# Performance work log

Hardware: AMD Instinct MI355X
Metric: run time of the kernel (lower is better)

## Reference

```python
import jax, jax.numpy as jnp
import numpy as np

EPS = 1e-5  # torch GroupNorm default eps


def _pairwise_sqdist(x, y):
    # squared euclidean distance matrix, clamped at 0 for numerical safety
    d = (jnp.sum(x * x, -1)[:, None] + jnp.sum(y * y, -1)[None, :]
         - 2.0 * (x @ y.T))
    return jnp.maximum(d, 0.0)


def _pc_normalize(ref, src):
    # jointly center and scale both clouds to the unit sphere
    pts = jnp.concatenate([ref, src], axis=0)
    centroid = pts.mean(axis=0, keepdims=True)
    pts = pts - centroid
    m = jnp.max(jnp.linalg.norm(pts, axis=1))
    pts = pts / m
    n_ref = ref.shape[0]
    return pts[:n_ref], pts[n_ref:]


def _group_norm(x, gamma, beta, groups):
    N, C = x.shape
    xg = x.reshape(N, groups, C // groups)
    mean = xg.mean(-1, keepdims=True)
    var = jnp.mean((xg - mean) ** 2, -1, keepdims=True)
    xn = ((xg - mean) / jnp.sqrt(var + EPS)).reshape(N, C)
    return xn * gamma + beta


def setup_inputs() -> dict:
    key = jax.random.key(0)
    ks = jax.random.split(key, 8)
    N_ref, N_src, D = 128, 128, 256
    points_c = jax.random.normal(ks[0], (N_ref + N_src, 3), jnp.float32)
    ref_feats = jax.random.normal(ks[1], (N_ref, D), jnp.float32)
    src_feats = jax.random.normal(ks[2], (N_src, D), jnp.float32)
    # normalized features, as the '_norm' names suggest
    ref_feats = ref_feats / jnp.linalg.norm(ref_feats, axis=-1, keepdims=True)
    src_feats = src_feats / jnp.linalg.norm(src_feats, axis=-1, keepdims=True)
    # a valid rigid transform: random rotation + small translation
    A = jax.random.normal(ks[3], (3, 3), jnp.float32)
    Q, _ = jnp.linalg.qr(A)
    trans = jnp.eye(4, dtype=jnp.float32)
    trans = trans.at[:3, :3].set(Q)
    trans = trans.at[:3, 3].set(jax.random.normal(ks[4], (3,), jnp.float32) * 0.1)
    s = 1.0 / np.sqrt(512)
    return {
        'points_c': points_c,
        'ref_feats_c_norm': ref_feats,
        'src_feats_c_norm': src_feats,
        'trans': trans,
        'W1': jax.random.normal(ks[5], (256, 512), jnp.float32) * s,
        'b1': jnp.zeros((256,), jnp.float32),
        'g1': jnp.ones((256,), jnp.float32),
        'bt1': jnp.zeros((256,), jnp.float32),
        'W2': jax.random.normal(ks[6], (128, 256), jnp.float32) * (1.0 / np.sqrt(256)),
        'b2': jnp.zeros((128,), jnp.float32),
        'g2': jnp.ones((128,), jnp.float32),
        'bt2': jnp.zeros((128,), jnp.float32),
        'W3': jax.random.normal(ks[7], (2, 128), jnp.float32) * (1.0 / np.sqrt(128)),
        'b3': jnp.zeros((2,), jnp.float32),
        'ref_length': 128,
    }


def reference(points_c, ref_feats_c_norm, src_feats_c_norm, trans,
              W1, b1, g1, bt1, W2, b2, g2, bt2, W3, b3, ref_length):
    GROUPS = 8
    ref_points = points_c[:ref_length]
    src_points = points_c[ref_length:]
    # apply rigid transform to src points
    src_points = src_points @ trans[:3, :3].T + trans[:3, 3]
    ref_n, src_n = _pc_normalize(ref_points, src_points)

    dist_mat = jnp.exp(-_pairwise_sqdist(ref_n, src_n))  # [Nr, Ns]
    match_idx_ref = jnp.argmax(dist_mat, axis=1)
    match_idx_src = jnp.argmax(dist_mat, axis=0)
    min_dist_ref = jnp.max(dist_mat, axis=1)
    min_dist_src = jnp.max(dist_mat, axis=0)

    feat_score_mat = ref_feats_c_norm @ src_feats_c_norm.T  # [Nr, Ns]
    feat_match_idx_ref = jnp.argmax(feat_score_mat, axis=1)
    feat_match_idx_src = jnp.argmax(feat_score_mat, axis=0)
    feat_match_ref = jnp.max(feat_score_mat, axis=1)
    feat_match_src = jnp.max(feat_score_mat, axis=0)

    r_idx = jnp.arange(feat_score_mat.shape[0])
    c_idx = jnp.arange(feat_score_mat.shape[1])
    feat_score_ref = feat_score_mat[r_idx, match_idx_ref]
    feat_score_src = feat_score_mat[match_idx_src, c_idx]
    dist_ref = dist_mat[r_idx, feat_match_idx_ref]
    dist_src = dist_mat[feat_match_idx_src, c_idx]

    min_dist = jnp.concatenate([min_dist_ref, min_dist_src])
    feat_score = jnp.concatenate([feat_score_ref, feat_score_src])
    perm_d = jnp.argsort(-min_dist)  # descending sort
    d_m = min_dist[perm_d] * feat_score[perm_d]

    match_feat = jnp.concatenate([feat_match_ref, feat_match_src])
    match_dist = jnp.concatenate([dist_ref, dist_src])
    perm_f = jnp.argsort(-match_feat)
    m_d = match_dist[perm_f] * match_feat[perm_f]

    geo_out = jnp.concatenate([d_m, m_d])[None, :]  # [1, 512]

    h = _group_norm(geo_out @ W1.T + b1, g1, bt1, GROUPS)
    h = jax.nn.relu(h)
    h = _group_norm(h @ W2.T + b2, g2, bt2, GROUPS)
    h = jax.nn.relu(h)
    return h @ W3.T + b3  # [1, num_classes]
```

## Files before the change

### kernel.cpp

```cpp
#include <hip/hip_runtime.h>
#include <math.h>

#define NREF 128
#define NSRC 128
#define DIM  256
#define EPS  1e-5f

__global__ __launch_bounds__(512) void feat_kernel(
    const float* __restrict__ ref_feats,
    const float* __restrict__ src_feats,
    float* __restrict__ feat_mat)
{
    __shared__ __align__(16) float refrow[DIM];
    const int i = blockIdx.x;
    const int t = threadIdx.x;
    if (t < 64) ((float4*)refrow)[t] = ((const float4*)(ref_feats + i * DIM))[t];
    __syncthreads();

    const int w = t >> 6, l = t & 63;
    const float4 r = ((const float4*)refrow)[l];

    for (int m = 0; m < 16; m += 2) {
        const int j0 = w * 16 + m;
        const int j1 = j0 + 1;
        const float4 a0 = ((const float4*)(src_feats + j0 * DIM))[l];
        const float4 a1 = ((const float4*)(src_feats + j1 * DIM))[l];
        float acc0 = a0.x * r.x + a0.y * r.y + a0.z * r.z + a0.w * r.w;
        float acc1 = a1.x * r.x + a1.y * r.y + a1.z * r.z + a1.w * r.w;
        for (int off = 32; off >= 1; off >>= 1) {
            acc0 += __shfl_down(acc0, off);
            acc1 += __shfl_down(acc1, off);
        }
        if (l == 0) {
            feat_mat[i * NSRC + j0] = acc0;
            feat_mat[i * NSRC + j1] = acc1;
        }
    }
}

__global__ __launch_bounds__(1024) void geo_kernel(
    const float* __restrict__ points_c,
    const float* __restrict__ trans,
    const float* __restrict__ feat_mat,
    float* __restrict__ geo_out)
{
    __shared__ float px[256], py[256], pz[256], nsq[256];
    __shared__ float wred[16];
    __shared__ float red[4];
    __shared__ float pvD[1024]; __shared__ int piD[1024];
    __shared__ float pvF[1024]; __shared__ int piF[1024];
    __shared__ float min_dist[256];   __shared__ int match_idx[256];
    __shared__ float match_feat[256]; __shared__ int feat_idx[256];
    __shared__ float feat_score[256], match_dist[256];
    __shared__ int prD[1024]; __shared__ int prF[1024];

    const int t    = threadIdx.x;
    const int wave = t >> 6;
    const int lane = t & 63;

    float x = 0.f, y = 0.f, z = 0.f;
    if (t < 256) {
        x = points_c[3 * t + 0];
        y = points_c[3 * t + 1];
        z = points_c[3 * t + 2];
        if (t >= NREF) {
            float nx = trans[0] * x + trans[1] * y + trans[2]  * z + trans[3];
            float ny = trans[4] * x + trans[5] * y + trans[6]  * z + trans[7];
            float nz = trans[8] * x + trans[9] * y + trans[10] * z + trans[11];
            x = nx; y = ny; z = nz;
        }
        float sx = x, sy = y, sz = z;
        for (int off = 32; off >= 1; off >>= 1) {
            sx += __shfl_down(sx, off);
            sy += __shfl_down(sy, off);
            sz += __shfl_down(sz, off);
        }
        if (lane == 0) {
            wred[wave]     = sx;
            wred[4 + wave] = sy;
            wred[8 + wave] = sz;
        }
    }
    __syncthreads();
    if (t == 0) {
        red[0] = (wred[0] + wred[1] + wred[2] + wred[3]) * (1.0f / 256.0f);
        red[1] = (wred[4] + wred[5] + wred[6] + wred[7]) * (1.0f / 256.0f);
        red[2] = (wred[8] + wred[9] + wred[10] + wred[11]) * (1.0f / 256.0f);
    }
    __syncthreads();

    if (t < 256) {
        x -= red[0]; y -= red[1]; z -= red[2];
        float n = x * x + y * y + z * z;
        float mx = n;
        for (int off = 32; off >= 1; off >>= 1)
            mx = fmaxf(mx, __shfl_down(mx, off));
        if (lane == 0) wred[wave] = mx;
    }
    __syncthreads();
    if (t == 0)
        red[3] = 1.0f / sqrtf(fmaxf(fmaxf(wred[0], wred[1]), fmaxf(wred[2], wred[3])));
    __syncthreads();
    if (t < 256) {
        const float inv = red[3];
        x *= inv; y *= inv; z *= inv;
        px[t] = x; py[t] = y; pz[t] = z;
        nsq[t] = x * x + y * y + z * z;
    }
    __syncthreads();

    {
        const int rc = t & 255, q = t >> 8;
        float bdv = -1.f; int bdi = 0;
        float bfv = -2.f; int bfi = 0;
        if (rc < 128) {
            const int i = rc;
            for (int m = 0; m < 32; ++m) {
                const int j = q * 32 + m;
                float d = nsq[i] + nsq[128 + j]
                        - 2.0f * (px[i] * px[128 + j] + py[i] * py[128 + j] + pz[i] * pz[128 + j]);
                d = fmaxf(d, 0.f);
                const float v = expf(-d);
                if (v > bdv) { bdv = v; bdi = j; }
                const float f = feat_mat[i * NSRC + j];
                if (f > bfv) { bfv = f; bfi = j; }
            }
        } else {
            const int j = rc - 128;
            for (int m = 0; m < 32; ++m) {
                const int i = q * 32 + m;
                float d = nsq[i] + nsq[128 + j]
                        - 2.0f * (px[i] * px[128 + j] + py[i] * py[128 + j] + pz[i] * pz[128 + j]);
                d = fmaxf(d, 0.f);
                const float v = expf(-d);
                if (v > bdv) { bdv = v; bdi = i; }
                const float f = feat_mat[i * NSRC + j];
                if (f > bfv) { bfv = f; bfi = i; }
            }
        }
        pvD[q * 256 + rc] = bdv; piD[q * 256 + rc] = bdi;
        pvF[q * 256 + rc] = bfv; piF[q * 256 + rc] = bfi;
    }
    __syncthreads();

    if (t < 256) {
        float bv = -1.f; int bi = 0;
        for (int q = 0; q < 4; ++q) {
            const float v = pvD[q * 256 + t];
            if (v > bv) { bv = v; bi = piD[q * 256 + t]; }
        }
        min_dist[t] = bv; match_idx[t] = bi;
        float fv = -2.f; int fi = 0;
        for (int q = 0; q < 4; ++q) {
            const float v = pvF[q * 256 + t];
            if (v > fv) { fv = v; fi = piF[q * 256 + t]; }
        }
        match_feat[t] = fv; feat_idx[t] = fi;
    }
    __syncthreads();

    if (t < 256) {
        if (t < NREF) {
            const int i = t;
            feat_score[t] = feat_mat[i * NSRC + match_idx[t]];
            const int j = feat_idx[t];
            float d = nsq[i] + nsq[128 + j]
                    - 2.0f * (px[i] * px[128 + j] + py[i] * py[128 + j] + pz[i] * pz[128 + j]);
            d = fmaxf(d, 0.f);
            match_dist[t] = expf(-d);
        } else {
            const int j = t - 128;
            feat_score[t] = feat_mat[match_idx[t] * NSRC + j];
            const int i = feat_idx[t];
            float d = nsq[i] + nsq[128 + j]
                    - 2.0f * (px[i] * px[128 + j] + py[i] * py[128 + j] + pz[i] * pz[128 + j]);
            d = fmaxf(d, 0.f);
            match_dist[t] = expf(-d);
        }
    }
    __syncthreads();

    {
        const int e = t & 255, q = t >> 8;
        const float v  = min_dist[e];
        const float wv = match_feat[e];
        int r1 = 0, r2 = 0;
        for (int m = 0; m < 64; ++m) {
            const int j = q * 64 + m;
            const float u  = min_dist[j];
            r1 += (u > v) || (u == v && j < e);
            const float uf = match_feat[j];
            r2 += (uf > wv) || (uf == wv && j < e);
        }
        prD[q * 256 + e] = r1;
        prF[q * 256 + e] = r2;
    }
    __syncthreads();
    if (t < 256) {
        const int r  = prD[t] + prD[256 + t] + prD[512 + t] + prD[768 + t];
        geo_out[r] = min_dist[t] * feat_score[t];
        const int rf = prF[t] + prF[256 + t] + prF[512 + t] + prF[768 + t];
        geo_out[256 + rf] = match_dist[t] * match_feat[t];
    }
}

__global__ __launch_bounds__(64) void mlp1_kernel(
    const float* __restrict__ geo,
    const float* __restrict__ W1, const float* __restrict__ b1,
    float* __restrict__ y1)
{
    const int c = blockIdx.x, l = threadIdx.x;
    const float4 ga = ((const float4*)geo)[l];
    const float4 gb = ((const float4*)geo)[64 + l];
    const float4* __restrict__ wrow = (const float4*)(W1 + c * 512);
    const float4 a = wrow[l];
    const float4 b = wrow[64 + l];
    float acc = a.x * ga.x + a.y * ga.y + a.z * ga.z + a.w * ga.w
              + b.x * gb.x + b.y * gb.y + b.z * gb.z + b.w * gb.w;
    acc += __shfl_down(acc, 32);
    acc += __shfl_down(acc, 16);
    acc += __shfl_down(acc, 8);
    acc += __shfl_down(acc, 4);
    acc += __shfl_down(acc, 2);
    acc += __shfl_down(acc, 1);
    if (l == 0) y1[c] = acc + b1[c];
}

__global__ __launch_bounds__(64) void mlp2_kernel(
    const float* __restrict__ y1,
    const float* __restrict__ g1, const float* __restrict__ bt1,
    const float* __restrict__ W2, const float* __restrict__ b2,
    float* __restrict__ y2)
{
    __shared__ __align__(16) float y1s[256];
    __shared__ float stats[16];
    const int c = blockIdx.x, l = threadIdx.x;
    ((float4*)y1s)[l] = ((const float4*)y1)[l];
    __syncthreads();
    if (l < 8) {
        float s = 0.f;
        for (int k = 0; k < 32; ++k) s += y1s[(l << 5) + k];
        const float mean = s * (1.0f / 32.0f);
        float q = 0.f;
        for (int k = 0; k < 32; ++k) { const float d = y1s[(l << 5) + k] - mean; q += d * d; }
        const float var = q * (1.0f / 32.0f);
        stats[l] = mean;
        stats[8 + l] = rsqrtf(var + EPS);
    }
    __syncthreads();
    const float4 gg = ((const float4*)g1)[l];
    const float4 bb = ((const float4*)bt1)[l];
    const int g = l >> 3;
    const float mean = stats[g], inv = stats[8 + g];
    const float4 yv = ((const float4*)y1s)[l];
    float4 h;
    h.x = fmaxf((yv.x - mean) * inv * gg.x + bb.x, 0.f);
    h.y = fmaxf((yv.y - mean) * inv * gg.y + bb.y, 0.f);
    h.z = fmaxf((yv.z - mean) * inv * gg.z + bb.z, 0.f);
    h.w = fmaxf((yv.w - mean) * inv * gg.w + bb.w, 0.f);
    const float4 wv = ((const float4*)(W2 + c * 256))[l];
    float acc = wv.x * h.x + wv.y * h.y + wv.z * h.z + wv.w * h.w;
    acc += __shfl_down(acc, 32);
    acc += __shfl_down(acc, 16);
    acc += __shfl_down(acc, 8);
    acc += __shfl_down(acc, 4);
    acc += __shfl_down(acc, 2);
    acc += __shfl_down(acc, 1);
    if (l == 0) y2[c] = acc + b2[c];
}

__global__ __launch_bounds__(128) void final_kernel(
    const float* __restrict__ y2,
    const float* __restrict__ g2, const float* __restrict__ bt2,
    const float* __restrict__ W3, const float* __restrict__ b3,
    float* __restrict__ out)
{
    __shared__ float y2s[128], h2[128];
    const int t = threadIdx.x;
    y2s[t] = y2[t];
    __syncthreads();
    {
        const int g = t >> 4;
        float s = 0.f;
        for (int k = 0; k < 16; ++k) s += y2s[(g << 4) + k];
        const float mean = s * (1.0f / 16.0f);
        float q = 0.f;
        for (int k = 0; k < 16; ++k) { const float d = y2s[(g << 4) + k] - mean; q += d * d; }
        const float var = q * (1.0f / 16.0f);
        const float xn = (y2s[t] - mean) * rsqrtf(var + EPS);
        h2[t] = fmaxf(xn * g2[t] + bt2[t], 0.f);
    }
    __syncthreads();
    const int wave = t >> 6, lane = t & 63;
    float acc = W3[wave * 128 + lane] * h2[lane]
              + W3[wave * 128 + 64 + lane] * h2[64 + lane];
    acc += __shfl_down(acc, 32);
    acc += __shfl_down(acc, 16);
    acc += __shfl_down(acc, 8);
    acc += __shfl_down(acc, 4);
    acc += __shfl_down(acc, 2);
    acc += __shfl_down(acc, 1);
    if (lane == 0) out[wave] = acc + b3[wave];
}

extern "C" void kernel_launch(void* const* d_in, const int* in_sizes, int n_in,
                              void* d_out, int out_size, void* d_ws, size_t ws_size,
                              hipStream_t stream)
{
    const float* points_c  = (const float*)d_in[0];
    const float* ref_feats = (const float*)d_in[1];
    const float* src_feats = (const float*)d_in[2];
    const float* trans     = (const float*)d_in[3];
    const float* W1  = (const float*)d_in[4];
    const float* b1  = (const float*)d_in[5];
    const float* g1  = (const float*)d_in[6];
    const float* bt1 = (const float*)d_in[7];
    const float* W2  = (const float*)d_in[8];
    const float* b2  = (const float*)d_in[9];
    const float* g2  = (const float*)d_in[10];
    const float* bt2 = (const float*)d_in[11];
    const float* W3  = (const float*)d_in[12];
    const float* b3  = (const float*)d_in[13];

    float* feat_mat = (float*)d_ws;
    float* geo = feat_mat;
    float* y1  = feat_mat + 512;
    float* y2  = feat_mat + 768;

    feat_kernel<<<dim3(NREF), dim3(512), 0, stream>>>(ref_feats, src_feats, feat_mat);
    geo_kernel<<<dim3(1), dim3(1024), 0, stream>>>(points_c, trans, feat_mat, geo);
    mlp1_kernel<<<dim3(256), dim3(64), 0, stream>>>(geo, W1, b1, y1);
    mlp2_kernel<<<dim3(128), dim3(64), 0, stream>>>(y1, g1, bt1, W2, b2, y2);
    final_kernel<<<dim3(1), dim3(128), 0, stream>>>(y2, g2, bt2, W3, b3, (float*)d_out);
}
```

Baseline: 104.8 us.

## Fuse five kernels into two: per-row/col side kernel and single-block MLP tail

Replaces the feature-matrix kernel, single-block geo kernel and three MLP kernels with two launches. A 256-block side kernel has each block handle one ref row or src column: it recomputes the normalized point cloud, computes its dot products and geometric scores, and reduces the argmaxes locally, so no feature matrix goes through global memory. A single 512-thread tail kernel does the rank-based sort and the whole MLP in shared memory. This cuts launch overhead and intermediate global traffic, at the cost of redundantly recomputing the centroid and scale per block and running the MLP matvecs on one CU.

```diff
diff --git a/kernel.cpp b/kernel.cpp
--- a/kernel.cpp
+++ b/kernel.cpp
@@ -6,57 +6,26 @@
 #define DIM  256
 #define EPS  1e-5f
 
-__global__ __launch_bounds__(512) void feat_kernel(
+__global__ __launch_bounds__(512) void side_kernel(
+    const float* __restrict__ points_c,
+    const float* __restrict__ trans,
     const float* __restrict__ ref_feats,
     const float* __restrict__ src_feats,
-    float* __restrict__ feat_mat)
-{
-    __shared__ __align__(16) float refrow[DIM];
-    const int i = blockIdx.x;
-    const int t = threadIdx.x;
-    if (t < 64) ((float4*)refrow)[t] = ((const float4*)(ref_feats + i * DIM))[t];
-    __syncthreads();
-
-    const int w = t >> 6, l = t & 63;
-    const float4 r = ((const float4*)refrow)[l];
-
-    for (int m = 0; m < 16; m += 2) {
-        const int j0 = w * 16 + m;
-        const int j1 = j0 + 1;
-        const float4 a0 = ((const float4*)(src_feats + j0 * DIM))[l];
-        const float4 a1 = ((const float4*)(src_feats + j1 * DIM))[l];
-        float acc0 = a0.x * r.x + a0.y * r.y + a0.z * r.z + a0.w * r.w;
-        float acc1 = a1.x * r.x + a1.y * r.y + a1.z * r.z + a1.w * r.w;
-        for (int off = 32; off >= 1; off >>= 1) {
-            acc0 += __shfl_down(acc0, off);
-            acc1 += __shfl_down(acc1, off);
-        }
-        if (l == 0) {
-            feat_mat[i * NSRC + j0] = acc0;
-            feat_mat[i * NSRC + j1] = acc1;
-        }
-    }
-}
-
-__global__ __launch_bounds__(1024) void geo_kernel(
-    const float* __restrict__ points_c,
-    const float* __restrict__ trans,
-    const float* __restrict__ feat_mat,
-    float* __restrict__ geo_out)
+    float* __restrict__ arrs)
 {
     __shared__ float px[256], py[256], pz[256], nsq[256];
-    __shared__ float wred[16];
+    __shared__ float wred[12];
     __shared__ float red[4];
-    __shared__ float pvD[1024]; __shared__ int piD[1024];
-    __shared__ float pvF[1024]; __shared__ int piF[1024];
-    __shared__ float min_dist[256];   __shared__ int match_idx[256];
-    __shared__ float match_feat[256]; __shared__ int feat_idx[256];
-    __shared__ float feat_score[256], match_dist[256];
-    __shared__ int prD[1024]; __shared__ int prF[1024];
-
-    const int t    = threadIdx.x;
-    const int wave = t >> 6;
-    const int lane = t & 63;
+    __shared__ float featLds[128];
+    __shared__ float cvD[8]; __shared__ int ciD[8];
+    __shared__ float cvF[8]; __shared__ int ciF[8];
+
+    const int b = blockIdx.x;
+    const int t = threadIdx.x;
+    const int w = t >> 6, l = t & 63;
+
+    const bool isRow = (b < NREF);
+    const int  me    = isRow ? b : (b - NREF);
 
     float x = 0.f, y = 0.f, z = 0.f;
     if (t < 256) {
@@ -69,17 +38,37 @@
             float nz = trans[8] * x + trans[9] * y + trans[10] * z + trans[11];
             x = nx; y = ny; z = nz;
         }
+    }
+
+    const float* __restrict__ myrow = (isRow ? ref_feats : src_feats) + me * DIM;
+    const float4* __restrict__ other = (const float4*)(isRow ? src_feats : ref_feats);
+    const float4 r = ((const float4*)myrow)[l];
+
+    float bfv = -2.f; int bfi = 0;
+    for (int m = 0; m < 16; m += 2) {
+        const int j0 = w * 16 + m, j1 = j0 + 1;
+        const float4 a0 = other[j0 * 64 + l];
+        const float4 a1 = other[j1 * 64 + l];
+        float acc0 = a0.x * r.x + a0.y * r.y + a0.z * r.z + a0.w * r.w;
+        float acc1 = a1.x * r.x + a1.y * r.y + a1.z * r.z + a1.w * r.w;
+        for (int off = 32; off >= 1; off >>= 1) {
+            acc0 += __shfl_xor(acc0, off);
+            acc1 += __shfl_xor(acc1, off);
+        }
+        if (l == 0) { featLds[j0] = acc0; featLds[j1] = acc1; }
+        if (acc0 > bfv) { bfv = acc0; bfi = j0; }
+        if (acc1 > bfv) { bfv = acc1; bfi = j1; }
+    }
+    if (l == 0) { cvF[w] = bfv; ciF[w] = bfi; }
+
+    if (t < 256) {
         float sx = x, sy = y, sz = z;
         for (int off = 32; off >= 1; off >>= 1) {
             sx += __shfl_down(sx, off);
             sy += __shfl_down(sy, off);
             sz += __shfl_down(sz, off);
         }
-        if (lane == 0) {
-            wred[wave]     = sx;
-            wred[4 + wave] = sy;
-            wred[8 + wave] = sz;
-        }
+        if (l == 0) { wred[w] = sx; wred[4 + w] = sy; wred[8 + w] = sz; }
     }
     __syncthreads();
     if (t == 0) {
@@ -88,14 +77,13 @@
         red[2] = (wred[8] + wred[9] + wred[10] + wred[11]) * (1.0f / 256.0f);
     }
     __syncthreads();
-
     if (t < 256) {
         x -= red[0]; y -= red[1]; z -= red[2];
         float n = x * x + y * y + z * z;
         float mx = n;
         for (int off = 32; off >= 1; off >>= 1)
             mx = fmaxf(mx, __shfl_down(mx, off));
-        if (lane == 0) wred[wave] = mx;
+        if (l == 0) wred[w] = mx;
     }
     __syncthreads();
     if (t == 0)
@@ -109,198 +97,163 @@
     }
     __syncthreads();
 
-    {
-        const int rc = t & 255, q = t >> 8;
-        float bdv = -1.f; int bdi = 0;
-        float bfv = -2.f; int bfi = 0;
-        if (rc < 128) {
-            const int i = rc;
-            for (int m = 0; m < 32; ++m) {
-                const int j = q * 32 + m;
-                float d = nsq[i] + nsq[128 + j]
-                        - 2.0f * (px[i] * px[128 + j] + py[i] * py[128 + j] + pz[i] * pz[128 + j]);
-                d = fmaxf(d, 0.f);
-                const float v = expf(-d);
-                if (v > bdv) { bdv = v; bdi = j; }
-                const float f = feat_mat[i * NSRC + j];
-                if (f > bfv) { bfv = f; bfi = j; }
-            }
-        } else {
-            const int j = rc - 128;
-            for (int m = 0; m < 32; ++m) {
-                const int i = q * 32 + m;
-                float d = nsq[i] + nsq[128 + j]
-                        - 2.0f * (px[i] * px[128 + j] + py[i] * py[128 + j] + pz[i] * pz[128 + j]);
-                d = fmaxf(d, 0.f);
-                const float v = expf(-d);
-                if (v > bdv) { bdv = v; bdi = i; }
-                const float f = feat_mat[i * NSRC + j];
-                if (f > bfv) { bfv = f; bfi = i; }
-            }
-        }
-        pvD[q * 256 + rc] = bdv; piD[q * 256 + rc] = bdi;
-        pvF[q * 256 + rc] = bfv; piF[q * 256 + rc] = bfi;
-    }
-    __syncthreads();
-
-    if (t < 256) {
+    float bdv = -1.f; int bdi = 0;
+    for (int m = 0; m < 16; ++m) {
+        const int jj = w * 16 + m;
+        const int i = isRow ? me : jj;
+        const int j = isRow ? jj : me;
+        float d = nsq[i] + nsq[128 + j]
+                - 2.0f * (px[i] * px[128 + j] + py[i] * py[128 + j] + pz[i] * pz[128 + j]);
+        d = fmaxf(d, 0.f);
+        const float v = expf(-d);
+        if (v > bdv) { bdv = v; bdi = jj; }
+    }
+    if (l == 0) { cvD[w] = bdv; ciD[w] = bdi; }
+    __syncthreads();
+
+    if (t == 0) {
         float bv = -1.f; int bi = 0;
-        for (int q = 0; q < 4; ++q) {
-            const float v = pvD[q * 256 + t];
-            if (v > bv) { bv = v; bi = piD[q * 256 + t]; }
-        }
-        min_dist[t] = bv; match_idx[t] = bi;
+        for (int q = 0; q < 8; ++q)
+            if (cvD[q] > bv) { bv = cvD[q]; bi = ciD[q]; }
         float fv = -2.f; int fi = 0;
-        for (int q = 0; q < 4; ++q) {
-            const float v = pvF[q * 256 + t];
-            if (v > fv) { fv = v; fi = piF[q * 256 + t]; }
-        }
-        match_feat[t] = fv; feat_idx[t] = fi;
-    }
-    __syncthreads();
-
-    if (t < 256) {
-        if (t < NREF) {
-            const int i = t;
-            feat_score[t] = feat_mat[i * NSRC + match_idx[t]];
-            const int j = feat_idx[t];
-            float d = nsq[i] + nsq[128 + j]
-                    - 2.0f * (px[i] * px[128 + j] + py[i] * py[128 + j] + pz[i] * pz[128 + j]);
-            d = fmaxf(d, 0.f);
-            match_dist[t] = expf(-d);
-        } else {
-            const int j = t - 128;
-            feat_score[t] = feat_mat[match_idx[t] * NSRC + j];
-            const int i = feat_idx[t];
-            float d = nsq[i] + nsq[128 + j]
-                    - 2.0f * (px[i] * px[128 + j] + py[i] * py[128 + j] + pz[i] * pz[128 + j]);
-            d = fmaxf(d, 0.f);
-            match_dist[t] = expf(-d);
-        }
-    }
-    __syncthreads();
-
-    {
-        const int e = t & 255, q = t >> 8;
-        const float v  = min_dist[e];
-        const float wv = match_feat[e];
-        int r1 = 0, r2 = 0;
-        for (int m = 0; m < 64; ++m) {
-            const int j = q * 64 + m;
-            const float u  = min_dist[j];
-            r1 += (u > v) || (u == v && j < e);
-            const float uf = match_feat[j];
-            r2 += (uf > wv) || (uf == wv && j < e);
-        }
-        prD[q * 256 + e] = r1;
-        prF[q * 256 + e] = r2;
-    }
-    __syncthreads();
-    if (t < 256) {
-        const int r  = prD[t] + prD[256 + t] + prD[512 + t] + prD[768 + t];
-        geo_out[r] = min_dist[t] * feat_score[t];
-        const int rf = prF[t] + prF[256 + t] + prF[512 + t] + prF[768 + t];
-        geo_out[256 + rf] = match_dist[t] * match_feat[t];
+        for (int q = 0; q < 8; ++q)
+            if (cvF[q] > fv) { fv = cvF[q]; fi = ciF[q]; }
+        const float fscore = featLds[bi];
+        const int i = isRow ? me : fi;
+        const int j = isRow ? fi : me;
+        float d = nsq[i] + nsq[128 + j]
+                - 2.0f * (px[i] * px[128 + j] + py[i] * py[128 + j] + pz[i] * pz[128 + j]);
+        d = fmaxf(d, 0.f);
+        const float mdist = expf(-d);
+        const int gi = isRow ? me : NREF + me;
+        arrs[gi]       = bv;
+        arrs[256 + gi] = fscore;
+        arrs[512 + gi] = fv;
+        arrs[768 + gi] = mdist;
     }
 }
 
-__global__ __launch_bounds__(64) void mlp1_kernel(
-    const float* __restrict__ geo,
+__global__ __launch_bounds__(512) void tail_kernel(
+    const float* __restrict__ arrs,
     const float* __restrict__ W1, const float* __restrict__ b1,
-    float* __restrict__ y1)
-{
-    const int c = blockIdx.x, l = threadIdx.x;
-    const float4 ga = ((const float4*)geo)[l];
-    const float4 gb = ((const float4*)geo)[64 + l];
-    const float4* __restrict__ wrow = (const float4*)(W1 + c * 512);
-    const float4 a = wrow[l];
-    const float4 b = wrow[64 + l];
-    float acc = a.x * ga.x + a.y * ga.y + a.z * ga.z + a.w * ga.w
-              + b.x * gb.x + b.y * gb.y + b.z * gb.z + b.w * gb.w;
-    acc += __shfl_down(acc, 32);
-    acc += __shfl_down(acc, 16);
-    acc += __shfl_down(acc, 8);
-    acc += __shfl_down(acc, 4);
-    acc += __shfl_down(acc, 2);
-    acc += __shfl_down(acc, 1);
-    if (l == 0) y1[c] = acc + b1[c];
-}
-
-__global__ __launch_bounds__(64) void mlp2_kernel(
-    const float* __restrict__ y1,
     const float* __restrict__ g1, const float* __restrict__ bt1,
     const float* __restrict__ W2, const float* __restrict__ b2,
-    float* __restrict__ y2)
-{
-    __shared__ __align__(16) float y1s[256];
-    __shared__ float stats[16];
-    const int c = blockIdx.x, l = threadIdx.x;
-    ((float4*)y1s)[l] = ((const float4*)y1)[l];
-    __syncthreads();
-    if (l < 8) {
-        float s = 0.f;
-        for (int k = 0; k < 32; ++k) s += y1s[(l << 5) + k];
-        const float mean = s * (1.0f / 32.0f);
-        float q = 0.f;
-        for (int k = 0; k < 32; ++k) { const float d = y1s[(l << 5) + k] - mean; q += d * d; }
-        const float var = q * (1.0f / 32.0f);
-        stats[l] = mean;
-        stats[8 + l] = rsqrtf(var + EPS);
-    }
-    __syncthreads();
-    const float4 gg = ((const float4*)g1)[l];
-    const float4 bb = ((const float4*)bt1)[l];
-    const int g = l >> 3;
-    const float mean = stats[g], inv = stats[8 + g];
-    const float4 yv = ((const float4*)y1s)[l];
-    float4 h;
-    h.x = fmaxf((yv.x - mean) * inv * gg.x + bb.x, 0.f);
-    h.y = fmaxf((yv.y - mean) * inv * gg.y + bb.y, 0.f);
-    h.z = fmaxf((yv.z - mean) * inv * gg.z + bb.z, 0.f);
-    h.w = fmaxf((yv.w - mean) * inv * gg.w + bb.w, 0.f);
-    const float4 wv = ((const float4*)(W2 + c * 256))[l];
-    float acc = wv.x * h.x + wv.y * h.y + wv.z * h.z + wv.w * h.w;
-    acc += __shfl_down(acc, 32);
-    acc += __shfl_down(acc, 16);
-    acc += __shfl_down(acc, 8);
-    acc += __shfl_down(acc, 4);
-    acc += __shfl_down(acc, 2);
-    acc += __shfl_down(acc, 1);
-    if (l == 0) y2[c] = acc + b2[c];
-}
-
-__global__ __launch_bounds__(128) void final_kernel(
-    const float* __restrict__ y2,
     const float* __restrict__ g2, const float* __restrict__ bt2,
     const float* __restrict__ W3, const float* __restrict__ b3,
     float* __restrict__ out)
 {
-    __shared__ float y2s[128], h2[128];
+    __shared__ __align__(16) float arrD[256], arrFS[256], arrMF[256], arrMD[256];
+    __shared__ __align__(16) float geoLds[512];
+    __shared__ __align__(16) float h1s[256];
+    __shared__ float y1s[256];
+    __shared__ float stats[16];
+    __shared__ float y2s[128], h2s[128];
+
     const int t = threadIdx.x;
-    y2s[t] = y2[t];
-    __syncthreads();
+    const int w = t >> 6, l = t & 63;
+
+    if (t < 256) {
+        arrD[t]  = arrs[t];
+        arrFS[t] = arrs[256 + t];
+        arrMF[t] = arrs[512 + t];
+        arrMD[t] = arrs[768 + t];
+    }
+    __syncthreads();
+
     {
+        const int e = t & 255;
+        const float* __restrict__ A = (t < 256) ? arrD : arrMF;
+        const float v = A[e];
+        int rk = 0;
+        for (int jb = 0; jb < 256; jb += 4) {
+            const float4 u = ((const float4*)A)[jb >> 2];
+            rk += (u.x > v) || (u.x == v && (jb + 0) < e);
+            rk += (u.y > v) || (u.y == v && (jb + 1) < e);
+            rk += (u.z > v) || (u.z == v && (jb + 2) < e);
+            rk += (u.w > v) || (u.w == v && (jb + 3) < e);
+        }
+        if (t < 256) geoLds[rk]       = arrD[e] * arrFS[e];
+        else         geoLds[256 + rk] = arrMD[e] * arrMF[e];
+    }
+    __syncthreads();
+
+    {
+        const float4 ga = ((const float4*)geoLds)[l];
+        const float4 gb = ((const float4*)geoLds)[64 + l];
+        for (int m = 0; m < 32; ++m) {
+            const int c = (w << 5) + m;
+            const float4* __restrict__ wrow = (const float4*)(W1 + c * 512);
+            const float4 a = wrow[l];
+            const float4 bq = wrow[64 + l];
+            float acc = a.x * ga.x + a.y * ga.y + a.z * ga.z + a.w * ga.w
+                      + bq.x * gb.x + bq.y * gb.y + bq.z * gb.z + bq.w * gb.w;
+            acc += __shfl_down(acc, 32);
+            acc += __shfl_down(acc, 16);
+            acc += __shfl_down(acc, 8);
+            acc += __shfl_down(acc, 4);
+            acc += __shfl_down(acc, 2);
+            acc += __shfl_down(acc, 1);
+            if (l == 0) y1s[c] = acc + b1[c];
+        }
+    }
+    __syncthreads();
+
+    if (t < 8) {
+        float s = 0.f;
+        for (int k = 0; k < 32; ++k) s += y1s[(t << 5) + k];
+        const float mean = s * (1.0f / 32.0f);
+        float q = 0.f;
+        for (int k = 0; k < 32; ++k) { const float d = y1s[(t << 5) + k] - mean; q += d * d; }
+        stats[t] = mean;
+        stats[8 + t] = rsqrtf(q * (1.0f / 32.0f) + EPS);
+    }
+    __syncthreads();
+    if (t < 256) {
+        const int g = t >> 5;
+        const float xn = (y1s[t] - stats[g]) * stats[8 + g];
+        h1s[t] = fmaxf(xn * g1[t] + bt1[t], 0.f);
+    }
+    __syncthreads();
+
+    {
+        const float4 hv = ((const float4*)h1s)[l];
+        for (int m = 0; m < 16; ++m) {
+            const int c = (w << 4) + m;
+            const float4 wv = ((const float4*)(W2 + c * 256))[l];
+            float acc = wv.x * hv.x + wv.y * hv.y + wv.z * hv.z + wv.w * hv.w;
+            acc += __shfl_down(acc, 32);
+            acc += __shfl_down(acc, 16);
+            acc += __shfl_down(acc, 8);
+            acc += __shfl_down(acc, 4);
+            acc += __shfl_down(acc, 2);
+            acc += __shfl_down(acc, 1);
+            if (l == 0) y2s[c] = acc + b2[c];
+        }
+    }
+    __syncthreads();
+
+    if (t < 128) {
         const int g = t >> 4;
         float s = 0.f;
         for (int k = 0; k < 16; ++k) s += y2s[(g << 4) + k];
         const float mean = s * (1.0f / 16.0f);
         float q = 0.f;
         for (int k = 0; k < 16; ++k) { const float d = y2s[(g << 4) + k] - mean; q += d * d; }
-        const float var = q * (1.0f / 16.0f);
-        const float xn = (y2s[t] - mean) * rsqrtf(var + EPS);
-        h2[t] = fmaxf(xn * g2[t] + bt2[t], 0.f);
-    }
-    __syncthreads();
-    const int wave = t >> 6, lane = t & 63;
-    float acc = W3[wave * 128 + lane] * h2[lane]
-              + W3[wave * 128 + 64 + lane] * h2[64 + lane];
-    acc += __shfl_down(acc, 32);
-    acc += __shfl_down(acc, 16);
-    acc += __shfl_down(acc, 8);
-    acc += __shfl_down(acc, 4);
-    acc += __shfl_down(acc, 2);
-    acc += __shfl_down(acc, 1);
-    if (lane == 0) out[wave] = acc + b3[wave];
+        const float xn = (y2s[t] - mean) * rsqrtf(q * (1.0f / 16.0f) + EPS);
+        h2s[t] = fmaxf(xn * g2[t] + bt2[t], 0.f);
+    }
+    __syncthreads();
+    if (t < 128) {
+        float acc = W3[w * 128 + l] * h2s[l]
+                  + W3[w * 128 + 64 + l] * h2s[64 + l];
+        acc += __shfl_down(acc, 32);
+        acc += __shfl_down(acc, 16);
+        acc += __shfl_down(acc, 8);
+        acc += __shfl_down(acc, 4);
+        acc += __shfl_down(acc, 2);
+        acc += __shfl_down(acc, 1);
+        if (l == 0) out[w] = acc + b3[w];
+    }
 }
 
 extern "C" void kernel_launch(void* const* d_in, const int* in_sizes, int n_in,
@@ -322,14 +275,10 @@
     const float* W3  = (const float*)d_in[12];
     const float* b3  = (const float*)d_in[13];
 
-    float* feat_mat = (float*)d_ws;
-    float* geo = feat_mat;
-    float* y1  = feat_mat + 512;
-    float* y2  = feat_mat + 768;
-
-    feat_kernel<<<dim3(NREF), dim3(512), 0, stream>>>(ref_feats, src_feats, feat_mat);
-    geo_kernel<<<dim3(1), dim3(1024), 0, stream>>>(points_c, trans, feat_mat, geo);
-    mlp1_kernel<<<dim3(256), dim3(64), 0, stream>>>(geo, W1, b1, y1);
-    mlp2_kernel<<<dim3(128), dim3(64), 0, stream>>>(y1, g1, bt1, W2, b2, y2);
-    final_kernel<<<dim3(1), dim3(128), 0, stream>>>(y2, g2, bt2, W3, b3, (float*)d_out);
+    float* arrs = (float*)d_ws;
+
+    side_kernel<<<dim3(256), dim3(512), 0, stream>>>(points_c, trans, ref_feats, src_feats, arrs);
+    tail_kernel<<<dim3(1), dim3(512), 0, stream>>>(arrs, W1, b1, g1, bt1,
+                                                   W2, b2, g2, bt2, W3, b3,
+                                                   (float*)d_out);
 }
```

New measurement: 129.1 us. 23.2% more time.
